# Kernel optimization log

Hardware: AMD Instinct MI355X
Metric: run time of the kernel (lower is better)

The kernel has to match this reference:

```python
import jax, jax.numpy as jnp
import numpy as np

B, S, D, H = 8, 1024, 1024, 16
DH = D // H
EPS = 1e-5


def _layernorm(x):
    # elementwise_affine=False LayerNorm, eps=1e-5
    m = jnp.mean(x, axis=-1, keepdims=True)
    v = jnp.var(x, axis=-1, keepdims=True)
    return (x - m) * jax.lax.rsqrt(v + EPS)


def setup_inputs() -> dict:
    key = jax.random.key(0)
    ks = jax.random.split(key, 11)
    s = 0.02
    return {
        "x": jax.random.normal(ks[0], (B, S, D), jnp.float32),
        "y": jax.random.normal(ks[1], (B, 1, D), jnp.float32),
        "w_adaln": jax.random.normal(ks[2], (6 * D, D), jnp.float32) * s,
        "b_adaln": jnp.zeros((6 * D,), jnp.float32),
        "w_qkv": jax.random.normal(ks[3], (3 * D, D), jnp.float32) * s,
        "w_proj": jax.random.normal(ks[4], (D, D), jnp.float32) * s,
        "b_proj": jnp.zeros((D,), jnp.float32),
        "w_fc1": jax.random.normal(ks[5], (4 * D, D), jnp.float32) * s,
        "b_fc1": jnp.zeros((4 * D,), jnp.float32),
        "w_fc2": jax.random.normal(ks[6], (D, 4 * D), jnp.float32) * s,
        "b_fc2": jnp.zeros((D,), jnp.float32),
    }


def reference(x, y, w_adaln, b_adaln, w_qkv, w_proj, b_proj, w_fc1, b_fc1, w_fc2, b_fc2):
    # adaLN-Zero modulation params from conditioning y: SiLU -> Linear -> 6 chunks
    mods = jax.nn.silu(y) @ w_adaln.T + b_adaln          # [B,1,6D]
    sh_a, sc_a, g_a, sh_m, sc_m, g_m = jnp.split(mods, 6, axis=-1)

    # --- attention branch ---
    xm = _layernorm(x) * (1.0 + sc_a) + sh_a             # modulate
    qkv = xm @ w_qkv.T                                   # [B,S,3D] (qkv_bias=False)
    q, k, v = [t.reshape(B, S, H, DH).transpose(0, 2, 1, 3) for t in jnp.split(qkv, 3, axis=-1)]
    scale = 1.0 / np.sqrt(DH)
    scores = jnp.einsum("bhqd,bhkd->bhqk", q, k) * scale  # unfused MATH-backend sdpa
    attn = jax.nn.softmax(scores, axis=-1)
    o = jnp.einsum("bhqk,bhkd->bhqd", attn, v)
    o = o.transpose(0, 2, 1, 3).reshape(B, S, D)
    o = o @ w_proj.T + b_proj
    x = x + g_a * o                                      # gated residual

    # --- MLP branch ---
    xm = _layernorm(x) * (1.0 + sc_m) + sh_m
    h = jax.nn.gelu(xm @ w_fc1.T + b_fc1, approximate=True)  # GELU(tanh)
    h = h @ w_fc2.T + b_fc2
    return x + g_m * h
```

## Files before the change

### kernel.cpp

```cpp
#include <hip/hip_runtime.h>

typedef __bf16 bf16;
typedef __attribute__((ext_vector_type(8))) __bf16 bf16x8;
typedef __attribute__((ext_vector_type(4))) __bf16 bf16x4;
typedef __attribute__((ext_vector_type(2))) __bf16 bf16x2;
typedef __attribute__((ext_vector_type(4))) float f32x4;

#define MFMA16(a, b, c) __builtin_amdgcn_mfma_f32_16x16x32_bf16((a), (b), (c), 0, 0, 0)

__device__ __forceinline__ float clampf(float v, float c) {
    return fminf(fmaxf(v, -c), c);
}

__device__ __forceinline__ void gload16(const void* g, void* l) {
    __builtin_amdgcn_global_load_lds((const __attribute__((address_space(1))) void*)g,
                                     (__attribute__((address_space(3))) void*)l, 16, 0, 0);
}

__launch_bounds__(256)
__global__ void cvt_kernel(const float* __restrict__ src, bf16* __restrict__ dst, int n4)
{
    int i = blockIdx.x * 256 + threadIdx.x;
    if (i < n4) {
        float4 v = ((const float4*)src)[i];
        bf16x4 o;
        o[0] = (bf16)v.x; o[1] = (bf16)v.y; o[2] = (bf16)v.z; o[3] = (bf16)v.w;
        ((bf16x4*)dst)[i] = o;
    }
}

__launch_bounds__(256)
__global__ void adaln_kernel(const float* __restrict__ y, const float* __restrict__ w,
                             const float* __restrict__ bias, float* __restrict__ mods)
{
    const int b = blockIdx.y;
    const int n = blockIdx.x * 256 + threadIdx.x;
    __shared__ float sy[1024];
    for (int i = threadIdx.x; i < 1024; i += 256) {
        float t = y[b * 1024 + i];
        sy[i] = t / (1.f + __expf(-t));
    }
    __syncthreads();
    const float* wr = w + (size_t)n * 1024;
    float acc = 0.f;
    for (int k = 0; k < 1024; k += 4) {
        float4 wv = *(const float4*)(wr + k);
        acc += sy[k] * wv.x + sy[k + 1] * wv.y + sy[k + 2] * wv.z + sy[k + 3] * wv.w;
    }
    mods[b * 6144 + n] = clampf(acc + bias[n], 64.f);
}

__launch_bounds__(256)
__global__ void ln_mod_kernel(const float* __restrict__ xin, const float* __restrict__ mods,
                              int shOff, int scOff, bf16* __restrict__ out)
{
    const int row = blockIdx.x;
    const int b = row >> 10;
    const int tid = threadIdx.x;
    const int wave = tid >> 6, lane = tid & 63;

    const float4 x4 = *((const float4*)xin + (size_t)row * 256 + tid);
    float v[4] = {x4.x, x4.y, x4.z, x4.w};

    float s = v[0] + v[1] + v[2] + v[3];
    float ss = v[0]*v[0] + v[1]*v[1] + v[2]*v[2] + v[3]*v[3];
#pragma unroll
    for (int o = 32; o > 0; o >>= 1) {
        s  += __shfl_xor(s, o, 64);
        ss += __shfl_xor(ss, o, 64);
    }
    __shared__ float red[8];
    if (lane == 0) { red[wave] = s; red[4 + wave] = ss; }
    __syncthreads();
    s  = red[0] + red[1] + red[2] + red[3];
    ss = red[4] + red[5] + red[6] + red[7];
    const float mean = s * (1.f / 1024.f);
    const float var  = ss * (1.f / 1024.f) - mean * mean;
    const float rstd = rsqrtf(fmaxf(var, 0.f) + 1e-5f);

    const float* mb = mods + b * 6144;
    bf16x4 o4;
#pragma unroll
    for (int j = 0; j < 4; ++j) {
        int c = tid * 4 + j;
        o4[j] = (bf16)clampf(((v[j] - mean) * rstd) * (1.f + mb[scOff + c]) + mb[shOff + c], 64.f);
    }
    *((bf16x4*)out + (size_t)row * 256 + tid) = o4;
}

template <int EPI>
__launch_bounds__(512, 2)
__global__ void gemm_np(const bf16* __restrict__ A, const bf16* __restrict__ W,
                        const float* __restrict__ bias, const float* __restrict__ mods,
                        int gateOff, const float* __restrict__ resid,
                        float* __restrict__ of, bf16* __restrict__ ob,
                        int N, int K, int nN, int GN, float clampV)
{
    __shared__ __align__(16) bf16 sm[3][3][8192];

    const int tid = threadIdx.x;
    const int wave = tid >> 6, lane = tid & 63, quad = lane >> 4, l16 = lane & 15;
    const int wm = wave >> 1, wn = wave & 1;

    const int xcd = (int)blockIdx.x & 7;
    const int p   = (int)blockIdx.x >> 3;
    const int nLoc = nN / GN;
    const int mLoc = ((int)gridDim.x >> 3) / nLoc;
    const int xm = xcd / GN, xn = xcd % GN;
    const int tileN = (xn * nLoc + p % nLoc) * 128;
    const int tileM = (xm * mLoc + p / nLoc) * 256;

    const int p0 = tid * 16;
    const int l0 = p0 ^ (((p0 >> 7) & 7) << 4);
    const int srow = l0 >> 7;
    const int scol = (l0 & 127) >> 1;
    const bf16* Ag  = A + (size_t)(tileM + srow) * K + scol;
    const bf16* Ag2 = Ag + (size_t)128 * K;
    const bf16* Wg  = W + (size_t)(tileN + srow) * K + scol;
    const size_t slotStep = (size_t)64 * K;

    const int xorv = (l16 & 7) << 4;
    const int cx0 = (quad * 16) ^ xorv;
    const int cx1 = (64 + quad * 16) ^ xorv;

    f32x4 acc[4][4] = {};
    bf16x8 af[4], bfr[4];

#define SPASS(r2, reg, src, p_, ts) \
    gload16((src) + (size_t)(p_) * slotStep + (size_t)(ts) * 64, \
            &sm[r2][reg][(p_) * 4096 + wave * 512])

#define RDNP(r, cx) do { \
        _Pragma("unroll") for (int q_ = 0; q_ < 4; ++q_) { \
            af[q_]  = *(const bf16x8*)((const char*)&sm[r][wm >> 1][0] + \
                        (((wm & 1) * 64 + q_ * 16 + l16) * 128) + (cx)); \
            bfr[q_] = *(const bf16x8*)((const char*)&sm[r][2][0] + \
                        ((wn * 64 + q_ * 16 + l16) * 128) + (cx)); \
        } \
    } while (0)

#define MMNP() do { \
        __builtin_amdgcn_s_setprio(1); \
        _Pragma("unroll") for (int m_ = 0; m_ < 4; ++m_) \
        _Pragma("unroll") for (int n_ = 0; n_ < 4; ++n_) \
            acc[m_][n_] = MFMA16(af[m_], bfr[n_], acc[m_][n_]); \
        __builtin_amdgcn_s_setprio(0); \
    } while (0)

#define BARF() do { __builtin_amdgcn_s_barrier(); asm volatile("" ::: "memory"); } while (0)
#define LGKM0() do { asm volatile("s_waitcnt lgkmcnt(0)" ::: "memory"); \
                     __builtin_amdgcn_sched_barrier(0); } while (0)
#define VMC6() do { asm volatile("s_waitcnt vmcnt(6)" ::: "memory"); \
                    __builtin_amdgcn_sched_barrier(0); } while (0)

#define KTILE(r, r2, T) do { \
        const int ts_ = ((T) + 2 < nkt) ? (T) + 2 : nkt - 1; \
         \
        RDNP(r, cx0); \
        SPASS(r2, 0, Ag, 0, ts_); SPASS(r2, 0, Ag, 1, ts_); SPASS(r2, 1, Ag2, 0, ts_); \
        BARF(); LGKM0(); \
        MMNP(); \
        BARF(); \
         \
        RDNP(r, cx1); \
        SPASS(r2, 1, Ag2, 1, ts_); SPASS(r2, 2, Wg, 0, ts_); SPASS(r2, 2, Wg, 1, ts_); \
        BARF(); LGKM0(); \
        MMNP(); \
        VMC6(); \
        BARF(); \
    } while (0)

    const int nkt = K >> 6;
    SPASS(0, 0, Ag, 0, 0); SPASS(0, 0, Ag, 1, 0); SPASS(0, 1, Ag2, 0, 0);
    SPASS(0, 1, Ag2, 1, 0); SPASS(0, 2, Wg, 0, 0); SPASS(0, 2, Wg, 1, 0);
    SPASS(1, 0, Ag, 0, 1); SPASS(1, 0, Ag, 1, 1); SPASS(1, 1, Ag2, 0, 1);
    SPASS(1, 1, Ag2, 1, 1); SPASS(1, 2, Wg, 0, 1); SPASS(1, 2, Wg, 1, 1);
    VMC6();
    BARF();

    for (int t = 0; t < nkt; t += 3) {
        KTILE(0, 2, t);
        if (t + 1 < nkt) KTILE(1, 0, t + 1);
        if (t + 2 < nkt) KTILE(2, 1, t + 2);
    }
    asm volatile("s_waitcnt vmcnt(0)" ::: "memory");

#undef SPASS
#undef RDNP
#undef MMNP
#undef BARF
#undef LGKM0
#undef VMC6
#undef KTILE

    const int rowB = tileM + wm * 64 + quad * 4;
    const int colB = tileN + wn * 64 + l16;
#pragma unroll
    for (int mt = 0; mt < 4; ++mt) {
#pragma unroll
        for (int nt = 0; nt < 4; ++nt) {
            const int col = colB + nt * 16;
#pragma unroll
            for (int i = 0; i < 4; ++i) {
                const int row = rowB + mt * 16 + i;
                float v = acc[mt][nt][i];
                if (EPI != 0) v += bias[col];
                if (EPI == 0) {
                    ob[(size_t)row * N + col] = (bf16)clampf(v, clampV);
                } else if (EPI == 1) {
                    const int bb = row >> 10;
                    const float g = mods[bb * 6144 + gateOff + col];
                    of[(size_t)row * N + col] =
                        clampf(resid[(size_t)row * N + col] + g * v, clampV);
                } else {
                    const float e = __expf(1.5957691216f * (v + 0.044715f * v * v * v));
                    const float tt = 1.f - 2.f / (e + 1.f);
                    ob[(size_t)row * N + col] = (bf16)clampf(0.5f * v * (1.f + tt), clampV);
                }
            }
        }
    }
}

template <int EPI>
__launch_bounds__(256)
__global__ void gemm_bt(const bf16* __restrict__ A, const float* __restrict__ W,
                        const float* __restrict__ bias, const float* __restrict__ mods,
                        int gateOff, const float* __restrict__ resid,
                        float* __restrict__ of, bf16* __restrict__ ob,
                        int M, int N, int K, float clampV)
{
    constexpr int LDT = 40;
    __shared__ bf16 As[128 * LDT];
    __shared__ bf16 Bs[128 * LDT];

    const int tid = threadIdx.x;
    const int wave = tid >> 6, lane = tid & 63, quad = lane >> 4, l16 = lane & 15;
    const int wrow = wave >> 1, wcol = wave & 1;
    const int tileM = blockIdx.y * 128, tileN = blockIdx.x * 128;
    const int sr = tid >> 2;
    const int sk = (tid & 3) * 8;

    const bf16*  Ag = A + (size_t)(tileM + sr) * K + sk;
    const float* Wg = W + (size_t)(tileN + sr) * K + sk;

    f32x4 acc[4][4] = {};

    for (int k0 = 0; k0 < K; k0 += 32) {
        bf16x8 a0 = *(const bf16x8*)(Ag + k0);
        bf16x8 a1 = *(const bf16x8*)(Ag + (size_t)64 * K + k0);
        float4 w0a = *(const float4*)(Wg + k0);
        float4 w0b = *(const float4*)(Wg + k0 + 4);
        float4 w1a = *(const float4*)(Wg + (size_t)64 * K + k0);
        float4 w1b = *(const float4*)(Wg + (size_t)64 * K + k0 + 4);
        bf16x8 b0, b1;
        b0[0] = (bf16)w0a.x; b0[1] = (bf16)w0a.y; b0[2] = (bf16)w0a.z; b0[3] = (bf16)w0a.w;
        b0[4] = (bf16)w0b.x; b0[5] = (bf16)w0b.y; b0[6] = (bf16)w0b.z; b0[7] = (bf16)w0b.w;
        b1[0] = (bf16)w1a.x; b1[1] = (bf16)w1a.y; b1[2] = (bf16)w1a.z; b1[3] = (bf16)w1a.w;
        b1[4] = (bf16)w1b.x; b1[5] = (bf16)w1b.y; b1[6] = (bf16)w1b.z; b1[7] = (bf16)w1b.w;
        *(bf16x8*)&As[sr * LDT + sk] = a0;
        *(bf16x8*)&As[(sr + 64) * LDT + sk] = a1;
        *(bf16x8*)&Bs[sr * LDT + sk] = b0;
        *(bf16x8*)&Bs[(sr + 64) * LDT + sk] = b1;
        __syncthreads();

        bf16x8 af[4], bfr[4];
#pragma unroll
        for (int mt = 0; mt < 4; ++mt)
            af[mt] = *(const bf16x8*)&As[(wrow * 64 + mt * 16 + l16) * LDT + quad * 8];
#pragma unroll
        for (int nt = 0; nt < 4; ++nt)
            bfr[nt] = *(const bf16x8*)&Bs[(wcol * 64 + nt * 16 + l16) * LDT + quad * 8];
#pragma unroll
        for (int mt = 0; mt < 4; ++mt)
#pragma unroll
            for (int nt = 0; nt < 4; ++nt)
                acc[mt][nt] = MFMA16(af[mt], bfr[nt], acc[mt][nt]);
        __syncthreads();
    }

#pragma unroll
    for (int mt = 0; mt < 4; ++mt) {
#pragma unroll
        for (int nt = 0; nt < 4; ++nt) {
            const int col = tileN + wcol * 64 + nt * 16 + l16;
#pragma unroll
            for (int i = 0; i < 4; ++i) {
                const int row = tileM + wrow * 64 + mt * 16 + quad * 4 + i;
                float v = acc[mt][nt][i];
                if (EPI != 0) v += bias[col];
                if (EPI == 0) {
                    ob[(size_t)row * N + col] = (bf16)clampf(v, clampV);
                } else if (EPI == 1) {
                    const int bb = row >> 10;
                    const float g = mods[bb * 6144 + gateOff + col];
                    of[(size_t)row * N + col] =
                        clampf(resid[(size_t)row * N + col] + g * v, clampV);
                } else {
                    const float e = __expf(1.5957691216f * (v + 0.044715f * v * v * v));
                    const float t = 1.f - 2.f / (e + 1.f);
                    ob[(size_t)row * N + col] = (bf16)clampf(0.5f * v * (1.f + t), clampV);
                }
            }
        }
    }
}

__launch_bounds__(256)
__global__ void attn_kernel(const bf16* __restrict__ qkv, bf16* __restrict__ o)
{
    const int bid = blockIdx.x;
    const int qt = bid >> 7;
    const int b  = (bid >> 4) & 7;
    const int h  = bid & 15;
    const int tid = threadIdx.x;
    const int wave = tid >> 6, lane = tid & 63, quad = lane >> 4, l16 = lane & 15;

    __shared__ bf16 Kl[64 * 72];
    __shared__ bf16 Vt[64 * 72];
    __shared__ bf16 Pl[4][32 * 72];

    const size_t basebs = (size_t)b * 1024 * 3072;
    const int qbase = qt * 128 + wave * 32;

    bf16x8 qf[2][2];
#pragma unroll
    for (int mt = 0; mt < 2; ++mt)
#pragma unroll
        for (int kk = 0; kk < 2; ++kk) {
            const int row = qbase + mt * 16 + l16;
            const int dh = kk * 32 + quad * 8;
            qf[mt][kk] = *(const bf16x8*)(qkv + basebs + (size_t)row * 3072 + h * 64 + dh);
        }

    const int kr = tid >> 2, kc = (tid & 3) * 16;
    const int vp = tid >> 3, vc = (tid & 7) * 8;
    const bf16* Kg = qkv + basebs + (size_t)kr * 3072 + 1024 + h * 64 + kc;
    const bf16* Vg = qkv + basebs + (size_t)(2 * vp) * 3072 + 2048 + h * 64 + vc;
    const size_t ktStep = (size_t)64 * 3072;

    bf16x8 k0 = *(const bf16x8*)Kg;
    bf16x8 k1 = *(const bf16x8*)(Kg + 8);
    bf16x8 v0 = *(const bf16x8*)Vg;
    bf16x8 v1 = *(const bf16x8*)(Vg + 3072);

    f32x4 oacc[2][4] = {};
    float lsum[2][4] = {};

    for (int kt = 0; kt < 16; ++kt) {
        *(bf16x8*)&Kl[kr * 72 + kc] = k0;
        *(bf16x8*)&Kl[kr * 72 + kc + 8] = k1;
#pragma unroll
        for (int j = 0; j < 8; ++j) {
            bf16x2 pr; pr[0] = v0[j]; pr[1] = v1[j];
            *(bf16x2*)&Vt[(vc + j) * 72 + 2 * vp] = pr;
        }
        __syncthreads();

        const size_t noff = (size_t)(kt < 15 ? kt + 1 : 15) * ktStep;
        k0 = *(const bf16x8*)(Kg + noff);
        k1 = *(const bf16x8*)(Kg + noff + 8);
        v0 = *(const bf16x8*)(Vg + noff);
        v1 = *(const bf16x8*)(Vg + noff + 3072);

        f32x4 s[2][4] = {};
#pragma unroll
        for (int kk = 0; kk < 2; ++kk)
#pragma unroll
            for (int nt = 0; nt < 4; ++nt) {
                bf16x8 kf = *(const bf16x8*)&Kl[(nt * 16 + l16) * 72 + kk * 32 + quad * 8];
#pragma unroll
                for (int mt = 0; mt < 2; ++mt)
                    s[mt][nt] = MFMA16(qf[mt][kk], kf, s[mt][nt]);
            }

#pragma unroll
        for (int mt = 0; mt < 2; ++mt)
#pragma unroll
            for (int nt = 0; nt < 4; ++nt)
#pragma unroll
                for (int i = 0; i < 4; ++i) {
                    float p = exp2f(fminf(s[mt][nt][i] * 0.18033688f, 43.f));
                    Pl[wave][(mt * 16 + quad * 4 + i) * 72 + nt * 16 + l16] = (bf16)p;
                    lsum[mt][i] += p;
                }

#pragma unroll
        for (int kk = 0; kk < 2; ++kk) {
            bf16x8 pf[2];
#pragma unroll
            for (int mt = 0; mt < 2; ++mt)
                pf[mt] = *(const bf16x8*)&Pl[wave][(mt * 16 + l16) * 72 + kk * 32 + quad * 8];
#pragma unroll
            for (int nt = 0; nt < 4; ++nt) {
                bf16x8 vf = *(const bf16x8*)&Vt[(nt * 16 + l16) * 72 + kk * 32 + quad * 8];
#pragma unroll
                for (int mt = 0; mt < 2; ++mt)
                    oacc[mt][nt] = MFMA16(pf[mt], vf, oacc[mt][nt]);
            }
        }
        __syncthreads();
    }

    bf16* ob = o + (size_t)b * 1024 * 1024 + h * 64;
#pragma unroll
    for (int mt = 0; mt < 2; ++mt)
#pragma unroll
        for (int i = 0; i < 4; ++i) {
            float l = lsum[mt][i];
#pragma unroll
            for (int off = 1; off < 16; off <<= 1) l += __shfl_xor(l, off, 64);
            const float inv = 1.f / fmaxf(l, 1e-20f);
            const int row = qbase + mt * 16 + quad * 4 + i;
#pragma unroll
            for (int nt = 0; nt < 4; ++nt)
                ob[(size_t)row * 1024 + nt * 16 + l16] = (bf16)clampf(oacc[mt][nt][i] * inv, 16.f);
        }
}

extern "C" void kernel_launch(void* const* d_in, const int* in_sizes, int n_in,
                              void* d_out, int out_size, void* d_ws, size_t ws_size,
                              hipStream_t stream)
{
    const float* x       = (const float*)d_in[0];
    const float* y       = (const float*)d_in[1];
    const float* w_adaln = (const float*)d_in[2];
    const float* b_adaln = (const float*)d_in[3];
    const float* w_qkv   = (const float*)d_in[4];
    const float* w_proj  = (const float*)d_in[5];
    const float* b_proj  = (const float*)d_in[6];
    const float* w_fc1   = (const float*)d_in[7];
    const float* b_fc1   = (const float*)d_in[8];
    const float* w_fc2   = (const float*)d_in[9];
    const float* b_fc2   = (const float*)d_in[10];
    float* out = (float*)d_out;

    char* ws = (char*)d_ws;
    float* mods = (float*)ws;
    bf16* bufA  = (bf16*)(ws + (1ull << 18));
    bf16* bufH  = (bf16*)(ws + (1ull << 18) + (1ull << 24));
    size_t off = (1ull << 18) + (1ull << 24) + (1ull << 26);
    bf16* wb_qkv  = (bf16*)(ws + off);               off += 6ull << 20;
    bf16* wb_proj = (bf16*)(ws + off);               off += 2ull << 20;
    bf16* wb_fc1  = (bf16*)(ws + off);               off += 8ull << 20;
    bf16* wb_fc2  = (bf16*)(ws + off);               off += 8ull << 20;
    const bool fast = ws_size >= off;

    adaln_kernel<<<dim3(24, 8), 256, 0, stream>>>(y, w_adaln, b_adaln, mods);
    ln_mod_kernel<<<8192, 256, 0, stream>>>(x, mods, 0, 1024, bufA);

    if (fast) {
        cvt_kernel<<<(3072 * 256 + 255) / 256, 256, 0, stream>>>(w_qkv, wb_qkv, 3072 * 256);
        cvt_kernel<<<(1024 * 256 + 255) / 256, 256, 0, stream>>>(w_proj, wb_proj, 1024 * 256);
        cvt_kernel<<<(4096 * 256 + 255) / 256, 256, 0, stream>>>(w_fc1, wb_fc1, 4096 * 256);
        cvt_kernel<<<(4096 * 256 + 255) / 256, 256, 0, stream>>>(w_fc2, wb_fc2, 4096 * 256);

        gemm_np<0><<<768, 512, 0, stream>>>(bufA, wb_qkv, nullptr, nullptr, 0,
                                            nullptr, nullptr, bufH, 3072, 1024, 24, 4, 64.f);
        attn_kernel<<<1024, 256, 0, stream>>>(bufH, bufA);
        gemm_np<1><<<256, 512, 0, stream>>>(bufA, wb_proj, b_proj, mods, 2048,
                                            x, out, nullptr, 1024, 1024, 8, 2, 64.f);
        ln_mod_kernel<<<8192, 256, 0, stream>>>(out, mods, 3072, 4096, bufA);
        gemm_np<2><<<1024, 512, 0, stream>>>(bufA, wb_fc1, b_fc1, nullptr, 0,
                                             nullptr, nullptr, bufH, 4096, 1024, 32, 4, 64.f);
        gemm_np<1><<<256, 512, 0, stream>>>(bufH, wb_fc2, b_fc2, mods, 5120,
                                            out, out, nullptr, 1024, 4096, 8, 4, 64.f);
    } else {
        gemm_bt<0><<<dim3(24, 64), 256, 0, stream>>>(bufA, w_qkv, nullptr, nullptr, 0,
                                                     nullptr, nullptr, bufH, 8192, 3072, 1024, 64.f);
        attn_kernel<<<1024, 256, 0, stream>>>(bufH, bufA);
        gemm_bt<1><<<dim3(8, 64), 256, 0, stream>>>(bufA, w_proj, b_proj, mods, 2048,
                                                    x, out, nullptr, 8192, 1024, 1024, 64.f);
        ln_mod_kernel<<<8192, 256, 0, stream>>>(out, mods, 3072, 4096, bufA);
        gemm_bt<2><<<dim3(32, 64), 256, 0, stream>>>(bufA, w_fc1, b_fc1, nullptr, 0,
                                                     nullptr, nullptr, bufH, 8192, 4096, 1024, 64.f);
        gemm_bt<1><<<dim3(8, 64), 256, 0, stream>>>(bufH, w_fc2, b_fc2, mods, 5120,
                                                    out, out, nullptr, 8192, 1024, 4096, 64.f);
    }
}
```

Before: 530.0 us.

## Double-buffer GEMM fragment registers to overlap LDS reads with MFMA

```diff
diff --git a/kernel.cpp b/kernel.cpp
--- a/kernel.cpp
+++ b/kernel.cpp
@@ -109,6 +109,7 @@
     const int xm = xcd / GN, xn = xcd % GN;
     const int tileN = (xn * nLoc + p % nLoc) * 128;
     const int tileM = (xm * mLoc + p / nLoc) * 256;
+    (void)mLoc;
 
     const int p0 = tid * 16;
     const int l0 = p0 ^ (((p0 >> 7) & 7) << 4);
@@ -124,49 +125,48 @@
     const int cx1 = (64 + quad * 16) ^ xorv;
 
     f32x4 acc[4][4] = {};
-    bf16x8 af[4], bfr[4];
+    bf16x8 afE[4], bfE[4], afO[4], bfO[4];
 
 #define SPASS(r2, reg, src, p_, ts) \
     gload16((src) + (size_t)(p_) * slotStep + (size_t)(ts) * 64, \
             &sm[r2][reg][(p_) * 4096 + wave * 512])
 
-#define RDNP(r, cx) do { \
+#define RDF(r, cx, afX, bfX) do { \
         _Pragma("unroll") for (int q_ = 0; q_ < 4; ++q_) { \
-            af[q_]  = *(const bf16x8*)((const char*)&sm[r][wm >> 1][0] + \
+            afX[q_] = *(const bf16x8*)((const char*)&sm[r][wm >> 1][0] + \
                         (((wm & 1) * 64 + q_ * 16 + l16) * 128) + (cx)); \
-            bfr[q_] = *(const bf16x8*)((const char*)&sm[r][2][0] + \
+            bfX[q_] = *(const bf16x8*)((const char*)&sm[r][2][0] + \
                         ((wn * 64 + q_ * 16 + l16) * 128) + (cx)); \
         } \
     } while (0)
 
-#define MMNP() do { \
+#define MMX(afX, bfX) do { \
         __builtin_amdgcn_s_setprio(1); \
         _Pragma("unroll") for (int m_ = 0; m_ < 4; ++m_) \
         _Pragma("unroll") for (int n_ = 0; n_ < 4; ++n_) \
-            acc[m_][n_] = MFMA16(af[m_], bfr[n_], acc[m_][n_]); \
+            acc[m_][n_] = MFMA16(afX[m_], bfX[n_], acc[m_][n_]); \
         __builtin_amdgcn_s_setprio(0); \
     } while (0)
 
+#define SB0() __builtin_amdgcn_sched_barrier(0)
 #define BARF() do { __builtin_amdgcn_s_barrier(); asm volatile("" ::: "memory"); } while (0)
-#define LGKM0() do { asm volatile("s_waitcnt lgkmcnt(0)" ::: "memory"); \
-                     __builtin_amdgcn_sched_barrier(0); } while (0)
-#define VMC6() do { asm volatile("s_waitcnt vmcnt(6)" ::: "memory"); \
-                    __builtin_amdgcn_sched_barrier(0); } while (0)
-
-#define KTILE(r, r2, T) do { \
+#define VMC6() do { asm volatile("s_waitcnt vmcnt(6)" ::: "memory"); SB0(); } while (0)
+#define VMC3() do { asm volatile("s_waitcnt vmcnt(3)" ::: "memory"); SB0(); } while (0)
+
+#define KTILE(r, rn, r2, T) do { \
         const int ts_ = ((T) + 2 < nkt) ? (T) + 2 : nkt - 1; \
          \
-        RDNP(r, cx0); \
+        RDF(r, cx1, afO, bfO); \
         SPASS(r2, 0, Ag, 0, ts_); SPASS(r2, 0, Ag, 1, ts_); SPASS(r2, 1, Ag2, 0, ts_); \
-        BARF(); LGKM0(); \
-        MMNP(); \
+        SB0(); \
+        MMX(afE, bfE); \
+        VMC3(); \
         BARF(); \
          \
-        RDNP(r, cx1); \
+        RDF(rn, cx0, afE, bfE); \
         SPASS(r2, 1, Ag2, 1, ts_); SPASS(r2, 2, Wg, 0, ts_); SPASS(r2, 2, Wg, 1, ts_); \
-        BARF(); LGKM0(); \
-        MMNP(); \
-        VMC6(); \
+        SB0(); \
+        MMX(afO, bfO); \
         BARF(); \
     } while (0)
 
@@ -177,20 +177,22 @@
     SPASS(1, 1, Ag2, 1, 1); SPASS(1, 2, Wg, 0, 1); SPASS(1, 2, Wg, 1, 1);
     VMC6();
     BARF();
+    RDF(0, cx0, afE, bfE);
 
     for (int t = 0; t < nkt; t += 3) {
-        KTILE(0, 2, t);
-        if (t + 1 < nkt) KTILE(1, 0, t + 1);
-        if (t + 2 < nkt) KTILE(2, 1, t + 2);
-    }
-    asm volatile("s_waitcnt vmcnt(0)" ::: "memory");
+        KTILE(0, 1, 2, t);
+        if (t + 1 < nkt) KTILE(1, 2, 0, t + 1);
+        if (t + 2 < nkt) KTILE(2, 0, 1, t + 2);
+    }
+    asm volatile("s_waitcnt vmcnt(0) lgkmcnt(0)" ::: "memory");
 
 #undef SPASS
-#undef RDNP
-#undef MMNP
+#undef RDF
+#undef MMX
+#undef SB0
 #undef BARF
-#undef LGKM0
 #undef VMC6
+#undef VMC3
 #undef KTILE
 
     const int rowB = tileM + wm * 64 + quad * 4;
```

Result: no change. 522.3 us (-1.5%).
